# Optimization experiments

Hardware: AMD Instinct MI355X
Metric: run time of the kernel (lower is better)

Reference implementation:

```python
import jax, jax.numpy as jnp
import numpy as np

B, L, H, V = 2048, 1024, 64, 64
LN_EPS = 1e-5
DELTA_EPS = 1e-6


def setup_inputs() -> dict:
    key = jax.random.key(0)
    ks = jax.random.split(key, 16)
    s = 0.05
    return {
        'seq': jax.random.randint(ks[0], (B, L), 0, V),
        'embed_W': jax.random.normal(ks[1], (V, H), jnp.float32),
        'ff_w1': jax.random.normal(ks[2], (H, 2 * H), jnp.float32) * s,
        'ff_b1': jnp.zeros((2 * H,), jnp.float32),
        'ff_w2': jax.random.normal(ks[3], (2 * H, H), jnp.float32) * s,
        'ff_b2': jnp.zeros((H,), jnp.float32),
        'ln_g': jnp.ones((H,), jnp.float32),
        'ln_b': jnp.zeros((H,), jnp.float32),
        'gate_w1': jax.random.normal(ks[4], (H, 16), jnp.float32) * s,
        'gate_b1': jnp.zeros((16,), jnp.float32),
        'gate_w2': jax.random.normal(ks[5], (16, 1), jnp.float32) * s,
        'gate_b2': jnp.zeros((1,), jnp.float32),
        'read_w': jax.random.normal(ks[6], (H, H), jnp.float32) * s,
        'read_b': jnp.zeros((H,), jnp.float32),
        'out_w': jax.random.normal(ks[7], (H, V), jnp.float32) * s,
        'out_b': jnp.zeros((V,), jnp.float32),
    }


def _layernorm(x, g, b):
    mu = jnp.mean(x, axis=-1, keepdims=True)
    var = jnp.var(x, axis=-1, keepdims=True)
    return (x - mu) * jax.lax.rsqrt(var + LN_EPS) * g + b


def reference(seq, embed_W, ff_w1, ff_b1, ff_w2, ff_b2, ln_g, ln_b,
              gate_w1, gate_b1, gate_w2, gate_b2, read_w, read_b, out_w, out_b):
    h = embed_W[seq]                                        # (B, L, H)
    ff = jnp.maximum(h @ ff_w1 + ff_b1, 0.0) @ ff_w2 + ff_b2
    h = _layernorm(h + ff, ln_g, ln_b)                      # (B, L, H)

    ks_seq = jnp.transpose(h[:, :-1, :], (1, 0, 2))         # (L-1, B, H) keys for scan

    def step(M, k):
        # k: (B, H); M: (B, H, H) fast-weight memory
        g = jax.nn.sigmoid(jnp.maximum(k @ gate_w1 + gate_b1, 0.0) @ gate_w2 + gate_b2)  # (B, 1)
        v_pred = jnp.einsum('bij,bj->bi', jax.lax.stop_gradient(M), k)
        denom = jnp.sum(k * k, axis=-1, keepdims=True) + DELTA_EPS
        dv = k - v_pred / denom                             # (B, H)
        dM = dv[:, :, None] * k[:, None, :]                 # outer product (B, H, H)
        return M + g[:, :, None] * dM, None

    M0 = jnp.zeros((h.shape[0], H, H), h.dtype)
    M, _ = jax.lax.scan(step, M0, ks_seq)

    q = h[:, -1, :]
    ctx = jnp.einsum('bij,bj->bi', M, q)                    # (B, H)
    logits = (ctx @ read_w + read_b) @ out_w + out_b        # (B, V)
    return logits
```

## Files before the change

kernel.cpp:

```cpp
#include <hip/hip_runtime.h>
#include <hip/hip_bf16.h>
#include <math.h>

#define Bsz 2048
#define Lsz 1024
#define Hsz 64
#define Vsz 64
#define SW  8

#define OFF_TABLE 0
#define OFF_G     4096
#define OFF_GC    8192
#define OFF_P     12288
#define OFF_WC    16384
#define OFF_GV    20480
#define OFF_C     20544
#define OFF_BC    20608

__global__ __launch_bounds__(128) void prep1_kernel(
    const float* __restrict__ embed_W, const float* __restrict__ ff_w1, const float* __restrict__ ff_b1,
    const float* __restrict__ ff_w2, const float* __restrict__ ff_b2, const float* __restrict__ ln_g,
    const float* __restrict__ ln_b, const float* __restrict__ gate_w1, const float* __restrict__ gate_b1,
    const float* __restrict__ gate_w2, const float* __restrict__ gate_b2, const float* __restrict__ read_w,
    const float* __restrict__ read_b, const float* __restrict__ out_w, const float* __restrict__ out_b,
    float* __restrict__ ws)
{
    const int tid = threadIdx.x;
    const int blk = blockIdx.x;
    if (blk < 64) {
        const int v = blk;
        __shared__ float z[128];
        __shared__ float hsh[64];
        const float* Ev = embed_W + (v << 6);
        float a = ff_b1[tid];
        #pragma unroll
        for (int i = 0; i < 64; ++i) a = fmaf(Ev[i], ff_w1[i * 128 + tid], a);
        z[tid] = fmaxf(a, 0.0f);
        __syncthreads();
        if (tid < 64) {
            float x = Ev[tid] + ff_b2[tid];
            #pragma unroll
            for (int j = 0; j < 128; ++j) x = fmaf(z[j], ff_w2[j * 64 + tid], x);
            float mu = x;
            #pragma unroll
            for (int off = 32; off > 0; off >>= 1) mu += __shfl_xor(mu, off);
            mu *= (1.0f / 64.0f);
            const float dd = x - mu;
            float var = dd * dd;
            #pragma unroll
            for (int off = 32; off > 0; off >>= 1) var += __shfl_xor(var, off);
            var *= (1.0f / 64.0f);
            const float rstd = rsqrtf(var + 1e-5f);
            const float hv = fmaf(dd * rstd, ln_g[tid], ln_b[tid]);
            ws[OFF_TABLE + (v << 6) + tid] = hv;
            hsh[tid] = hv;
            float dn = hv * hv;
            #pragma unroll
            for (int off = 32; off > 0; off >>= 1) dn += __shfl_xor(dn, off);
            dn += 1e-6f;
            float a2 = 0.0f;
            if (tid < 16) {
                float um = gate_b1[tid];
                #pragma unroll
                for (int i = 0; i < 64; ++i) um = fmaf(hsh[i], gate_w1[i * 16 + tid], um);
                a2 = fmaxf(um, 0.0f) * gate_w2[tid];
            }
            #pragma unroll
            for (int off = 8; off > 0; off >>= 1) a2 += __shfl_xor(a2, off);
            if (tid == 0) {
                a2 += gate_b2[0];
                const float g = 1.0f / (1.0f + expf(-a2));
                ws[OFF_GV + v] = g;
                ws[OFF_C + v]  = g / dn;
            }
        }
    } else if (blk < 128) {
        const int j = blk - 64;
        if (tid < 64) {
            float a = 0.0f;
            #pragma unroll
            for (int m = 0; m < 64; ++m) a = fmaf(read_w[(j << 6) + m], out_w[(m << 6) + tid], a);
            ws[OFF_WC + (j << 6) + tid] = a;
        }
    } else {
        if (tid < 64) {
            float a = out_b[tid];
            #pragma unroll
            for (int jj = 0; jj < 64; ++jj) a = fmaf(read_b[jj], out_w[(jj << 6) + tid], a);
            ws[OFF_BC + tid] = a;
        }
    }
}

__global__ __launch_bounds__(64) void prep2_kernel(float* __restrict__ ws)
{
    const int tid = threadIdx.x;
    const int blk = blockIdx.x;
    if (blk < 64) {
        const int v = blk;
        __shared__ float tT[65 * 64];
        for (int idx = tid; idx < 4096; idx += 64) {
            const int w = idx >> 6, j = idx & 63;
            tT[j * 65 + w] = ws[OFF_TABLE + idx];
        }
        __syncthreads();
        const float cv = ws[OFF_C + v];
        float a = 0.0f;
        #pragma unroll
        for (int j = 0; j < 64; ++j) a = fmaf(tT[j * 65 + v], tT[j * 65 + tid], a);
        ws[OFF_G  + (v << 6) + tid] = a;
        ws[OFF_GC + (v << 6) + tid] = cv * a;
    } else {
        const int v = blk - 64;
        float a = 0.0f;
        #pragma unroll
        for (int j = 0; j < 64; ++j)
            a = fmaf(ws[OFF_TABLE + (v << 6) + j], ws[OFF_WC + (j << 6) + tid], a);
        ws[OFF_P + (v << 6) + tid] = a;
    }
}

__global__ __launch_bounds__(SW * 64) void scan_kernel(const int* __restrict__ seq,
                                                       const float* __restrict__ ws,
                                                       float* __restrict__ out)
{
    __shared__ float ldsGc[65 * 64];
    __shared__ float ldsP[4096];
    __shared__ int   toks[SW][1024];
    __shared__ float sbuf[SW][64];
    __shared__ float ldsg[64];
    __shared__ float ldsbc[64];

    const int tid  = threadIdx.x;
    const int wave = tid >> 6;
    const int lane = tid & 63;

    for (int i = tid; i < 4096; i += SW * 64) {
        ldsGc[i] = ws[OFF_GC + i];
        ldsP[i]  = ws[OFF_P + i];
    }
    if (tid < 64) {
        ldsGc[4096 + tid] = 0.0f;
        ldsg[tid]  = ws[OFF_GV + tid];
        ldsbc[tid] = ws[OFF_BC + tid];
    }
    const int b = blockIdx.x * SW + wave;
    const int* row = seq + (size_t)b * Lsz;
    {
        int4* dst = (int4*)toks[wave];
        const int4* src = (const int4*)row;
        for (int i = lane; i < 256; i += 64) dst[i] = src[i];
    }
    __syncthreads();

    const int tokL = toks[wave][1023];
    toks[wave][1023] = 64;
    float D = ws[OFF_G + (tokL << 6) + lane];
    float u = 0.0f;

    int   tkA[16], tkB[16];
    float gcA[16], gcB[16];

    int tokvA = toks[wave][1008 + lane];
    #pragma unroll
    for (int k = 0; k < 16; ++k) {
        tkA[k] = __builtin_amdgcn_readlane(tokvA, 15 - k) & 127;
        gcA[k] = ldsGc[(tkA[k] << 6) + lane];
    }
    int tokvB = toks[wave][992 + lane];

    for (int t0 = 1023; t0 > 0; t0 -= 32) {
        #pragma unroll
        for (int k = 0; k < 16; ++k) {
            tkB[k] = __builtin_amdgcn_readlane(tokvB, 15 - k) & 127;
            gcB[k] = ldsGc[(tkB[k] << 6) + lane];
        }
        {
            const int base = t0 - 47;
            tokvA = toks[wave][(base < 0 ? 0 : base) + lane];
        }
        #pragma unroll
        for (int k = 0; k < 16; ++k) {
            const int tok = tkA[k];
            const float d = __int_as_float(
                __builtin_amdgcn_readlane(__float_as_int(D), tok));
            u += (lane == tok) ? d : 0.0f;
            D = fmaf(-d, gcA[k], D);
        }
        #pragma unroll
        for (int k = 0; k < 16; ++k) {
            tkA[k] = __builtin_amdgcn_readlane(tokvA, 15 - k) & 127;
            gcA[k] = ldsGc[(tkA[k] << 6) + lane];
        }
        {
            const int base = t0 - 63;
            tokvB = toks[wave][(base < 0 ? 0 : base) + lane];
        }
        #pragma unroll
        for (int k = 0; k < 16; ++k) {
            const int tok = tkB[k];
            const float d = __int_as_float(
                __builtin_amdgcn_readlane(__float_as_int(D), tok));
            u += (lane == tok) ? d : 0.0f;
            D = fmaf(-d, gcB[k], D);
        }
    }

    sbuf[wave][lane] = ldsg[lane] * u;
    float acc = ldsbc[lane];
    #pragma unroll 8
    for (int v = 0; v < 64; ++v)
        acc = fmaf(sbuf[wave][v], ldsP[(v << 6) + lane], acc);
    out[(size_t)b * 64 + lane] = acc;
}

extern "C" void kernel_launch(void* const* d_in, const int* in_sizes, int n_in,
                              void* d_out, int out_size, void* d_ws, size_t ws_size,
                              hipStream_t stream) {
    const int*   seq     = (const int*)  d_in[0];
    const float* embed_W = (const float*)d_in[1];
    const float* ff_w1   = (const float*)d_in[2];
    const float* ff_b1   = (const float*)d_in[3];
    const float* ff_w2   = (const float*)d_in[4];
    const float* ff_b2   = (const float*)d_in[5];
    const float* ln_g    = (const float*)d_in[6];
    const float* ln_b    = (const float*)d_in[7];
    const float* gate_w1 = (const float*)d_in[8];
    const float* gate_b1 = (const float*)d_in[9];
    const float* gate_w2 = (const float*)d_in[10];
    const float* gate_b2 = (const float*)d_in[11];
    const float* read_w  = (const float*)d_in[12];
    const float* read_b  = (const float*)d_in[13];
    const float* out_w   = (const float*)d_in[14];
    const float* out_b   = (const float*)d_in[15];
    float* ws  = (float*)d_ws;
    float* out = (float*)d_out;

    hipLaunchKernelGGL(prep1_kernel, dim3(129), dim3(128), 0, stream,
                       embed_W, ff_w1, ff_b1, ff_w2, ff_b2, ln_g, ln_b,
                       gate_w1, gate_b1, gate_w2, gate_b2, read_w, read_b,
                       out_w, out_b, ws);
    hipLaunchKernelGGL(prep2_kernel, dim3(128), dim3(64), 0, stream, ws);
    hipLaunchKernelGGL(scan_kernel, dim3(Bsz / SW), dim3(SW * 64), 0, stream,
                       seq, ws, out);
}
```

Measured before the change: 137.3 us.

## Keep packed tokens in registers and drop per-wave LDS token staging

The scan kernel now loads each row's tokens straight into registers as int4, packs four 7-bit tokens per int, and pulls them out with readlane. This removes the 32KB LDS token buffer and its reloads. The gate vector is folded into the output projection table in prep2, and the G table is rebuilt from Gc times the inverse coefficient, which cuts LDS footprint and some global tables. Less LDS should raise occupancy, at the cost of more scalar readlane and bit-extract work inside the serial loop.

```diff
diff --git a/kernel.cpp b/kernel.cpp
--- a/kernel.cpp
+++ b/kernel.cpp
@@ -1,21 +1,22 @@
 #include <hip/hip_runtime.h>
-#include <hip/hip_bf16.h>
 #include <math.h>
 
 #define Bsz 2048
 #define Lsz 1024
-#define Hsz 64
-#define Vsz 64
 #define SW  8
 
-#define OFF_TABLE 0
-#define OFF_G     4096
-#define OFF_GC    8192
-#define OFF_P     12288
-#define OFF_WC    16384
-#define OFF_GV    20480
-#define OFF_C     20544
-#define OFF_BC    20608
+#define OFF_GC  0
+#define OFF_PG  4160
+#define OFF_H   8256
+#define OFF_WC  12352
+#define OFF_GV  16448
+#define OFF_CI  16512
+#define OFF_C   16576
+#define OFF_BC  16640
+
+__device__ __forceinline__ float __rlf(float v, int i) {
+    return __int_as_float(__builtin_amdgcn_readlane(__float_as_int(v), i));
+}
 
 __global__ __launch_bounds__(128) void prep1_kernel(
     const float* __restrict__ embed_W, const float* __restrict__ ff_w1, const float* __restrict__ ff_b1,
@@ -52,8 +53,8 @@
             var *= (1.0f / 64.0f);
             const float rstd = rsqrtf(var + 1e-5f);
             const float hv = fmaf(dd * rstd, ln_g[tid], ln_b[tid]);
-            ws[OFF_TABLE + (v << 6) + tid] = hv;
             hsh[tid] = hv;
+            ws[OFF_H + (v << 6) + tid] = hv;
             float dn = hv * hv;
             #pragma unroll
             for (int off = 32; off > 0; off >>= 1) dn += __shfl_xor(dn, off);
@@ -71,7 +72,8 @@
                 a2 += gate_b2[0];
                 const float g = 1.0f / (1.0f + expf(-a2));
                 ws[OFF_GV + v] = g;
-                ws[OFF_C + v]  = g / dn;
+                ws[OFF_C  + v] = g / dn;
+                ws[OFF_CI + v] = dn / g;
             }
         }
     } else if (blk < 128) {
@@ -96,27 +98,28 @@
 {
     const int tid = threadIdx.x;
     const int blk = blockIdx.x;
+    if (blk == 128) { ws[OFF_GC + 64 * 64 + tid] = 0.0f; return; }
+    __shared__ float tT[65 * 64];
+    for (int idx = tid; idx < 4096; idx += 64) {
+        const int w = idx >> 6, j = idx & 63;
+        tT[j * 65 + w] = ws[OFF_H + idx];
+    }
+    __syncthreads();
     if (blk < 64) {
         const int v = blk;
-        __shared__ float tT[65 * 64];
-        for (int idx = tid; idx < 4096; idx += 64) {
-            const int w = idx >> 6, j = idx & 63;
-            tT[j * 65 + w] = ws[OFF_TABLE + idx];
-        }
-        __syncthreads();
         const float cv = ws[OFF_C + v];
         float a = 0.0f;
         #pragma unroll
         for (int j = 0; j < 64; ++j) a = fmaf(tT[j * 65 + v], tT[j * 65 + tid], a);
-        ws[OFF_G  + (v << 6) + tid] = a;
         ws[OFF_GC + (v << 6) + tid] = cv * a;
     } else {
         const int v = blk - 64;
+        const float gv = ws[OFF_GV + v];
         float a = 0.0f;
         #pragma unroll
         for (int j = 0; j < 64; ++j)
-            a = fmaf(ws[OFF_TABLE + (v << 6) + j], ws[OFF_WC + (j << 6) + tid], a);
-        ws[OFF_P + (v << 6) + tid] = a;
+            a = fmaf(tT[j * 65 + v], ws[OFF_WC + (j << 6) + tid], a);
+        ws[OFF_PG + (v << 6) + tid] = gv * a;
     }
 }
 
@@ -125,92 +128,98 @@
                                                        float* __restrict__ out)
 {
     __shared__ float ldsGc[65 * 64];
-    __shared__ float ldsP[4096];
-    __shared__ int   toks[SW][1024];
-    __shared__ float sbuf[SW][64];
-    __shared__ float ldsg[64];
-    __shared__ float ldsbc[64];
+    __shared__ float ldsPg[64 * 64];
 
     const int tid  = threadIdx.x;
     const int wave = tid >> 6;
     const int lane = tid & 63;
-
-    for (int i = tid; i < 4096; i += SW * 64) {
-        ldsGc[i] = ws[OFF_GC + i];
-        ldsP[i]  = ws[OFF_P + i];
-    }
-    if (tid < 64) {
-        ldsGc[4096 + tid] = 0.0f;
-        ldsg[tid]  = ws[OFF_GV + tid];
-        ldsbc[tid] = ws[OFF_BC + tid];
-    }
-    const int b = blockIdx.x * SW + wave;
-    const int* row = seq + (size_t)b * Lsz;
+    const int b    = blockIdx.x * SW + wave;
+
+    const int4* ts = (const int4*)(seq + (size_t)b * Lsz);
+    const int4 q0 = ts[lane], q1 = ts[64 + lane], q2 = ts[128 + lane], q3 = ts[192 + lane];
+
     {
-        int4* dst = (int4*)toks[wave];
-        const int4* src = (const int4*)row;
-        for (int i = lane; i < 256; i += 64) dst[i] = src[i];
-    }
+        const float4* s1 = (const float4*)(ws + OFF_GC);
+        float4* d1 = (float4*)ldsGc;
+        for (int i = tid; i < 1040; i += SW * 64) d1[i] = s1[i];
+        const float4* s2 = (const float4*)(ws + OFF_PG);
+        float4* d2 = (float4*)ldsPg;
+        for (int i = tid; i < 1024; i += SW * 64) d2[i] = s2[i];
+    }
+
+    int tv0 = q0.x | (q0.y << 8) | (q0.z << 16) | (q0.w << 24);
+    int tv1 = q1.x | (q1.y << 8) | (q1.z << 16) | (q1.w << 24);
+    int tv2 = q2.x | (q2.y << 8) | (q2.z << 16) | (q2.w << 24);
+    int tv3 = q3.x | (q3.y << 8) | (q3.z << 16) | (q3.w << 24);
+
+    const int tokL = (__builtin_amdgcn_readlane(tv3, 63) >> 24) & 0x7F;
+    if (lane == 63) tv3 = (tv3 & 0x00FFFFFF) | (64 << 24);
+
     __syncthreads();
 
-    const int tokL = toks[wave][1023];
-    toks[wave][1023] = 64;
-    float D = ws[OFF_G + (tokL << 6) + lane];
+    float D = ldsGc[(tokL << 6) + lane] * ws[OFF_CI + tokL];
     float u = 0.0f;
 
-    int   tkA[16], tkB[16];
-    float gcA[16], gcB[16];
-
-    int tokvA = toks[wave][1008 + lane];
+    int   tk1[8], tk0[8], nk1[8], nk0[8];
+    float gA[8], gB[8];
+
+    auto EXT = [&](int wh, int wl, int* tk) {
+        tk[0] = (wh >> 24) & 0x7F; tk[1] = (wh >> 16) & 0x7F;
+        tk[2] = (wh >>  8) & 0x7F; tk[3] =  wh        & 0x7F;
+        tk[4] = (wl >> 24) & 0x7F; tk[5] = (wl >> 16) & 0x7F;
+        tk[6] = (wl >>  8) & 0x7F; tk[7] =  wl        & 0x7F;
+    };
+    auto ISSUE = [&](const int* tk, float* g) {
+        #pragma unroll
+        for (int k = 0; k < 8; ++k) g[k] = ldsGc[(tk[k] << 6) + lane];
+    };
+    auto STEP = [&](const int* tk, const float* g) {
+        #pragma unroll
+        for (int k = 0; k < 8; ++k) {
+            const float d = __rlf(D, tk[k]);
+            u += (lane == tk[k]) ? d : 0.0f;
+            D = fmaf(-d, g[k], D);
+        }
+    };
+
+    EXT(__builtin_amdgcn_readlane(tv3, 63), __builtin_amdgcn_readlane(tv3, 62), tk1);
+    EXT(__builtin_amdgcn_readlane(tv3, 61), __builtin_amdgcn_readlane(tv3, 60), tk0);
+    ISSUE(tk1, gA);
+
     #pragma unroll
-    for (int k = 0; k < 16; ++k) {
-        tkA[k] = __builtin_amdgcn_readlane(tokvA, 15 - k) & 127;
-        gcA[k] = ldsGc[(tkA[k] << 6) + lane];
-    }
-    int tokvB = toks[wave][992 + lane];
-
-    for (int t0 = 1023; t0 > 0; t0 -= 32) {
-        #pragma unroll
-        for (int k = 0; k < 16; ++k) {
-            tkB[k] = __builtin_amdgcn_readlane(tokvB, 15 - k) & 127;
-            gcB[k] = ldsGc[(tkB[k] << 6) + lane];
-        }
-        {
-            const int base = t0 - 47;
-            tokvA = toks[wave][(base < 0 ? 0 : base) + lane];
-        }
-        #pragma unroll
-        for (int k = 0; k < 16; ++k) {
-            const int tok = tkA[k];
-            const float d = __int_as_float(
-                __builtin_amdgcn_readlane(__float_as_int(D), tok));
-            u += (lane == tok) ? d : 0.0f;
-            D = fmaf(-d, gcA[k], D);
-        }
-        #pragma unroll
-        for (int k = 0; k < 16; ++k) {
-            tkA[k] = __builtin_amdgcn_readlane(tokvA, 15 - k) & 127;
-            gcA[k] = ldsGc[(tkA[k] << 6) + lane];
-        }
-        {
-            const int base = t0 - 63;
-            tokvB = toks[wave][(base < 0 ? 0 : base) + lane];
-        }
-        #pragma unroll
-        for (int k = 0; k < 16; ++k) {
-            const int tok = tkB[k];
-            const float d = __int_as_float(
-                __builtin_amdgcn_readlane(__float_as_int(D), tok));
-            u += (lane == tok) ? d : 0.0f;
-            D = fmaf(-d, gcB[k], D);
-        }
-    }
-
-    sbuf[wave][lane] = ldsg[lane] * u;
-    float acc = ldsbc[lane];
-    #pragma unroll 8
+    for (int p = 3; p >= 0; --p) {
+        const int tvp = (p == 3) ? tv3 : (p == 2) ? tv2 : (p == 1) ? tv1 : tv0;
+        for (int uu = 15; uu >= 1; --uu) {
+            ISSUE(tk0, gB);
+            STEP(tk1, gA);
+            EXT(__builtin_amdgcn_readlane(tvp, 4 * uu - 1),
+                __builtin_amdgcn_readlane(tvp, 4 * uu - 2), nk1);
+            EXT(__builtin_amdgcn_readlane(tvp, 4 * uu - 3),
+                __builtin_amdgcn_readlane(tvp, 4 * uu - 4), nk0);
+            ISSUE(nk1, gA);
+            STEP(tk0, gB);
+            #pragma unroll
+            for (int k = 0; k < 8; ++k) { tk1[k] = nk1[k]; tk0[k] = nk0[k]; }
+        }
+        ISSUE(tk0, gB);
+        STEP(tk1, gA);
+        if (p > 0) {
+            const int tvn = (p == 3) ? tv2 : (p == 2) ? tv1 : tv0;
+            EXT(__builtin_amdgcn_readlane(tvn, 63), __builtin_amdgcn_readlane(tvn, 62), nk1);
+            EXT(__builtin_amdgcn_readlane(tvn, 61), __builtin_amdgcn_readlane(tvn, 60), nk0);
+            ISSUE(nk1, gA);
+            STEP(tk0, gB);
+            #pragma unroll
+            for (int k = 0; k < 8; ++k) { tk1[k] = nk1[k]; tk0[k] = nk0[k]; }
+        } else {
+            STEP(tk0, gB);
+        }
+    }
+
+    float acc = ws[OFF_BC + lane];
+    #pragma unroll 16
     for (int v = 0; v < 64; ++v)
-        acc = fmaf(sbuf[wave][v], ldsP[(v << 6) + lane], acc);
+        acc = fmaf(__rlf(u, v), ldsPg[(v << 6) + lane], acc);
     out[(size_t)b * 64 + lane] = acc;
 }
 
@@ -240,7 +249,7 @@
                        embed_W, ff_w1, ff_b1, ff_w2, ff_b2, ln_g, ln_b,
                        gate_w1, gate_b1, gate_w2, gate_b2, read_w, read_b,
                        out_w, out_b, ws);
-    hipLaunchKernelGGL(prep2_kernel, dim3(128), dim3(64), 0, stream, ws);
+    hipLaunchKernelGGL(prep2_kernel, dim3(129), dim3(64), 0, stream, ws);
     hipLaunchKernelGGL(scan_kernel, dim3(Bsz / SW), dim3(SW * 64), 0, stream,
                        seq, ws, out);
 }
```

Measured after the change: 136.9 us. No clear change (-0.2%).
